# Kernel optimization log

Hardware: AMD Instinct MI355X
Metric: run time of the kernel (lower is better)

Reference implementation:

```python
import jax, jax.numpy as jnp
import numpy as np

D_MODEL = 1024
NUM_HEADS = 16


def setup_inputs() -> dict:
    key = jax.random.key(0)
    ks = jax.random.split(key, 9)
    B, S, D = 4, 1024, D_MODEL
    scale = 1.0 / np.sqrt(D)
    inp = {
        "query": jax.random.normal(ks[0], (B, S, D), dtype=jnp.float32),
        "key": jax.random.normal(ks[1], (B, S, D), dtype=jnp.float32),
        "value": jax.random.normal(ks[2], (B, S, D), dtype=jnp.float32),
        # causal mask: 1 = attend, 0 = blocked (masked_fill where mask==0)
        "mask": jnp.tril(jnp.ones((S, S), dtype=jnp.int32))[None, None, :, :],
        "Wq": jax.random.normal(ks[3], (D, D), dtype=jnp.float32) * scale,
        "Wk": jax.random.normal(ks[4], (D, D), dtype=jnp.float32) * scale,
        "Wv": jax.random.normal(ks[5], (D, D), dtype=jnp.float32) * scale,
        "Wo": jax.random.normal(ks[6], (D, D), dtype=jnp.float32) * scale,
        "bo": jnp.zeros((D,), dtype=jnp.float32),
    }
    return inp


def reference(query, key, value, mask, Wq, Wk, Wv, Wo, bo):
    B, S, D = query.shape
    H = NUM_HEADS
    dk = D // H
    # torch Linear: y = x @ W.T  (bias=False for q/k/v)
    def proj(x, W):
        return (x @ W.T).reshape(B, S, H, dk).transpose(0, 2, 1, 3)  # [B,H,S,dk]

    Q = proj(query, Wq)
    K = proj(key, Wk)
    V = proj(value, Wv)

    scores = jnp.einsum("bhqd,bhkd->bhqk", Q, K) / jnp.sqrt(
        jnp.asarray(dk, dtype=jnp.float32)
    )
    scores = jnp.where(mask == 0, jnp.asarray(-1e9, scores.dtype), scores)
    attn = jax.nn.softmax(scores, axis=-1)
    out = jnp.einsum("bhqk,bhkd->bhqd", attn, V)  # [B,H,S,dk]
    out = out.transpose(0, 2, 1, 3).reshape(B, S, D)
    return out @ Wo.T + bo
```

## Files before the change

### kernel.cpp

```cpp
#include <hip/hip_runtime.h>

typedef __bf16 bf16x8 __attribute__((ext_vector_type(8)));
typedef short  s16x8  __attribute__((ext_vector_type(8)));
typedef float  f32x4  __attribute__((ext_vector_type(4)));
typedef float  f32x16 __attribute__((ext_vector_type(16)));
typedef unsigned int   u32x4 __attribute__((ext_vector_type(4)));
typedef unsigned short u16x4 __attribute__((ext_vector_type(4)));

#define NH   16
#define HD   64
#define SEQ  1024
#define DM   1024
#define NB   4
#define MTOT 4096

#define SCALE_L2E 0.1803368801111204f

__device__ __forceinline__ unsigned short f2bf(float f) {
    unsigned u = __builtin_bit_cast(unsigned, f);
    u += 0x7FFFu + ((u >> 16) & 1u);
    return (unsigned short)(u >> 16);
}

__device__ __forceinline__ s16x8 cvt8(f32x4 a, f32x4 b) {
    s16x8 r;
    r[0] = (short)f2bf(a[0]); r[1] = (short)f2bf(a[1]);
    r[2] = (short)f2bf(a[2]); r[3] = (short)f2bf(a[3]);
    r[4] = (short)f2bf(b[0]); r[5] = (short)f2bf(b[1]);
    r[6] = (short)f2bf(b[2]); r[7] = (short)f2bf(b[3]);
    return r;
}

__device__ __forceinline__ unsigned short bfbits(float x) {
    __bf16 h = (__bf16)x;
    return __builtin_bit_cast(unsigned short, h);
}
__device__ __forceinline__ float bf2f(unsigned short b) {
    unsigned u = (unsigned)b << 16;
    return __builtin_bit_cast(float, u);
}
__device__ __forceinline__ unsigned pk2(float a, float b) {
    return (unsigned)bfbits(a) | ((unsigned)bfbits(b) << 16);
}

__device__ __forceinline__ void gl16(const void* g, void* l) {
    __builtin_amdgcn_global_load_lds(
        (const __attribute__((address_space(1))) unsigned int*)g,
        (__attribute__((address_space(3))) unsigned int*)l, 16, 0, 0);
}

__global__ __launch_bounds__(256)
void cvt_kernel(const float* __restrict__ q, const float* __restrict__ k,
                const float* __restrict__ v, const float* __restrict__ wq,
                const float* __restrict__ wk, const float* __restrict__ wv,
                const float* __restrict__ wo,
                unsigned short* __restrict__ dq, unsigned short* __restrict__ dk,
                unsigned short* __restrict__ dv, unsigned short* __restrict__ dwq,
                unsigned short* __restrict__ dwk, unsigned short* __restrict__ dwv,
                unsigned short* __restrict__ dwo)
{
    const int id = blockIdx.x;
    const float* s; unsigned short* d; int off; float scl = 1.0f;
    if (id < 6144) {
        const int t = id >> 11; off = id & 2047;
        s = (t == 0) ? q : (t == 1) ? k : v;
        d = (t == 0) ? dq : (t == 1) ? dk : dv;
    } else {
        const int w = (id - 6144) >> 9; off = (id - 6144) & 511;
        s = (w == 0) ? wq : (w == 1) ? wk : (w == 2) ? wv : wo;
        d = (w == 0) ? dwq : (w == 1) ? dwk : (w == 2) ? dwv : dwo;
        if (w == 0) scl = SCALE_L2E;
    }
    const int idx = off * 2048 + threadIdx.x * 8;
    const f32x4* sp = (const f32x4*)(s + idx);
    *(s16x8*)(d + idx) = cvt8(sp[0] * scl, sp[1] * scl);
}

__device__ __forceinline__ void stage128x64(const unsigned short* __restrict__ src,
                                            int row0, int k0, char* lds, int tid)
{
    const int wv  = tid >> 6;
    const int row = tid >> 3;
    const int scx = ((tid & 7) * 16) ^ ((row & 7) << 4);
    #pragma unroll
    for (int i = 0; i < 4; ++i) {
        const char* g = (const char*)(src + (size_t)(row0 + i * 32 + row) * DM + k0) + scx;
        gl16(g, lds + i * 4096 + wv * 1024);
    }
}

__device__ __forceinline__ void stage_half(const unsigned short* __restrict__ src,
                                           int grow0, int k0, char* ldsdst, int tid)
{
    const int wv  = tid >> 6;
    const int row = tid >> 3;
    const int scx = ((tid & 7) * 16) ^ ((row & 7) << 4);
    gl16((const char*)(src + (size_t)(grow0 + row) * DM + k0) + scx,
         ldsdst + wv * 1024);
    gl16((const char*)(src + (size_t)(grow0 + 64 + row) * DM + k0) + scx,
         ldsdst + 8192 + wv * 1024);
}

__device__ __forceinline__ bf16x8 ldfrag(const char* base, int row, int cb) {
    return __builtin_bit_cast(bf16x8,
        *(const s16x8*)(base + row * 128 + (cb ^ ((row & 7) << 4))));
}

__global__ __launch_bounds__(512, 2)
void proj_kernel(const unsigned short* __restrict__ Xq,
                 const unsigned short* __restrict__ Xk,
                 const unsigned short* __restrict__ Xv,
                 const unsigned short* __restrict__ Wq,
                 const unsigned short* __restrict__ Wk,
                 const unsigned short* __restrict__ Wv,
                 unsigned short* __restrict__ Qo, unsigned short* __restrict__ Ko,
                 unsigned short* __restrict__ VTo)
{
    __shared__ char smem[147456];

    const int bid = blockIdx.x;
    const int swz = (bid & 7) * 24 + (bid >> 3);
    const int which = swz >> 6;
    const int rem   = swz & 63;
    const int m0 = (rem >> 2) * 256, n0 = (rem & 3) * 256;

    const unsigned short* X = (which == 0) ? Xq : (which == 1) ? Xk : Xv;
    const unsigned short* W = (which == 0) ? Wq : (which == 1) ? Wk : Wv;

    const int tid = threadIdx.x, lane = tid & 63, wv = tid >> 6;
    const int wrB = (wv >> 2) * 128;
    const int wcB = (wv & 3) * 64;
    const int fr = lane & 15, hi = lane >> 4, r4 = hi * 4;

    f32x4 acc[8][4];
    #pragma unroll
    for (int i = 0; i < 8; ++i)
        #pragma unroll
        for (int j = 0; j < 4; ++j) acc[i][j] = (f32x4){0.f, 0.f, 0.f, 0.f};

    stage_half(X, m0,       0, smem +     0, tid);
    stage_half(X, m0 + 128, 0, smem + 16384, tid);
    stage_half(W, n0,       0, smem + 32768, tid);
    stage_half(W, n0 + 128, 0, smem + 49152, tid);

    for (int t = 0; t < 16; ++t) {
        const char* Abuf = smem + (t & 1) * 65536;
        const char* Bbuf = Abuf + 32768;
        char* nb = smem + ((t & 1) ^ 1) * 65536;
        const int kn = (t + 1) * 64;

        bf16x8 af[2][4], bf01[2][2], bf23[2][2];

        if (t < 15) {
            stage_half(X, m0, kn, nb, tid);
            asm volatile("s_waitcnt vmcnt(2)" ::: "memory");
        } else {
            asm volatile("s_waitcnt vmcnt(0)" ::: "memory");
        }
        __builtin_amdgcn_s_barrier();
        __builtin_amdgcn_sched_barrier(0);
        #pragma unroll
        for (int ks = 0; ks < 2; ++ks) {
            const int cb = ks * 64 + hi * 16;
            #pragma unroll
            for (int mt = 0; mt < 4; ++mt) af[ks][mt] = ldfrag(Abuf, wrB + mt * 16 + fr, cb);
            #pragma unroll
            for (int nt = 0; nt < 2; ++nt) bf01[ks][nt] = ldfrag(Bbuf, wcB + nt * 16 + fr, cb);
        }
        __builtin_amdgcn_s_setprio(1);
        #pragma unroll
        for (int ks = 0; ks < 2; ++ks)
            #pragma unroll
            for (int mt = 0; mt < 4; ++mt)
                #pragma unroll
                for (int nt = 0; nt < 2; ++nt)
                    acc[mt][nt] = __builtin_amdgcn_mfma_f32_16x16x32_bf16(
                        af[ks][mt], bf01[ks][nt], acc[mt][nt], 0, 0, 0);
        __builtin_amdgcn_s_setprio(0);

        __builtin_amdgcn_s_barrier();
        __builtin_amdgcn_sched_barrier(0);
        #pragma unroll
        for (int ks = 0; ks < 2; ++ks) {
            const int cb = ks * 64 + hi * 16;
            #pragma unroll
            for (int nt = 0; nt < 2; ++nt) bf23[ks][nt] = ldfrag(Bbuf, wcB + 32 + nt * 16 + fr, cb);
        }
        if (t < 15) stage_half(X, m0 + 128, kn, nb + 16384, tid);
        __builtin_amdgcn_s_setprio(1);
        #pragma unroll
        for (int ks = 0; ks < 2; ++ks)
            #pragma unroll
            for (int mt = 0; mt < 4; ++mt)
                #pragma unroll
                for (int nt = 0; nt < 2; ++nt)
                    acc[mt][nt + 2] = __builtin_amdgcn_mfma_f32_16x16x32_bf16(
                        af[ks][mt], bf23[ks][nt], acc[mt][nt + 2], 0, 0, 0);
        __builtin_amdgcn_s_setprio(0);

        __builtin_amdgcn_s_barrier();
        __builtin_amdgcn_sched_barrier(0);
        #pragma unroll
        for (int ks = 0; ks < 2; ++ks) {
            const int cb = ks * 64 + hi * 16;
            #pragma unroll
            for (int mt = 0; mt < 4; ++mt) af[ks][mt] = ldfrag(Abuf, wrB + 64 + mt * 16 + fr, cb);
        }
        if (t < 15) stage_half(W, n0, kn, nb + 32768, tid);
        __builtin_amdgcn_s_setprio(1);
        #pragma unroll
        for (int ks = 0; ks < 2; ++ks)
            #pragma unroll
            for (int mt = 0; mt < 4; ++mt)
                #pragma unroll
                for (int nt = 0; nt < 2; ++nt)
                    acc[mt + 4][nt] = __builtin_amdgcn_mfma_f32_16x16x32_bf16(
                        af[ks][mt], bf01[ks][nt], acc[mt + 4][nt], 0, 0, 0);
        __builtin_amdgcn_s_setprio(0);

        __builtin_amdgcn_s_barrier();
        __builtin_amdgcn_sched_barrier(0);
        if (t < 15) stage_half(W, n0 + 128, kn, nb + 49152, tid);
        __builtin_amdgcn_s_setprio(1);
        #pragma unroll
        for (int ks = 0; ks < 2; ++ks)
            #pragma unroll
            for (int mt = 0; mt < 4; ++mt)
                #pragma unroll
                for (int nt = 0; nt < 2; ++nt)
                    acc[mt + 4][nt + 2] = __builtin_amdgcn_mfma_f32_16x16x32_bf16(
                        af[ks][mt], bf23[ks][nt], acc[mt + 4][nt + 2], 0, 0, 0);
        __builtin_amdgcn_s_setprio(0);
    }

    __syncthreads();

    unsigned short* sE = (unsigned short*)(smem + wv * 18432);
    #pragma unroll
    for (int mt = 0; mt < 8; ++mt)
        #pragma unroll
        for (int nt = 0; nt < 4; ++nt)
            #pragma unroll
            for (int r = 0; r < 4; ++r) {
                const int row = mt * 16 + r4 + r;
                const int col = nt * 16 + fr;
                sE[row * 72 + (col ^ (((row >> 3) & 7) << 3))] = f2bf(acc[mt][nt][r]);
            }
    asm volatile("s_waitcnt lgkmcnt(0)" ::: "memory");

    const int hB    = (n0 + wcB) >> 6;
    const int sbase = m0 + wrB;
    const int bb    = sbase >> 10;
    const int srow0 = sbase & 1023;

    if (which < 2) {
        unsigned short* QK = ((which == 0) ? Qo : Ko)
            + (((size_t)(bb * NH + hB)) * SEQ + srow0) * HD;
        #pragma unroll
        for (int it = 0; it < 16; ++it) {
            const int idx = it * 64 + lane;
            const int row = idx >> 3, c = idx & 7;
            s16x8 v = *(const s16x8*)&sE[row * 72 + ((c ^ ((row >> 3) & 7)) * 8)];
            *(s16x8*)(QK + (size_t)row * HD + c * 8) = v;
        }
    } else {
        const int t0 = srow0 >> 6;
        unsigned short* VD = VTo + (size_t)(bb * NH + hB) * (SEQ * HD)
                                 + (size_t)t0 * 4096;
        #pragma unroll
        for (int it = 0; it < 16; ++it) {
            const int tt = it >> 3, r = it & 7;
            const int sb = tt * 64 + (r >> 1) * 16 + (lane >> 5) * 8;
            const int d  = (lane & 31) + (r & 1) * 32;
            s16x8 v;
            #pragma unroll
            for (int j = 0; j < 8; ++j) {
                const int row = sb + j;
                v[j] = (short)sE[row * 72 + (d ^ (((row >> 3) & 7) << 3))];
            }
            *(s16x8*)(VD + (size_t)(tt * 8 + r) * 512 + lane * 8) = v;
        }
    }
}

#define GEMM_K_LOOP(SRC_A, SRC_B)                                              \
    stage128x64(SRC_A, m0, 0, sA[0], tid);                                     \
    stage128x64(SRC_B, n0, 0, sB[0], tid);                                     \
    for (int kt = 0; kt < 16; ++kt) {                                          \
        const int cur = kt & 1;                                                \
        if (kt < 15) {                                                         \
            stage128x64(SRC_A, m0, (kt + 1) * 64, sA[cur ^ 1], tid);           \
            stage128x64(SRC_B, n0, (kt + 1) * 64, sB[cur ^ 1], tid);           \
            asm volatile("s_waitcnt vmcnt(8)" ::: "memory");                   \
        } else {                                                               \
            asm volatile("s_waitcnt vmcnt(0)" ::: "memory");                   \
        }                                                                      \
        __builtin_amdgcn_s_barrier();                                          \
        __builtin_amdgcn_sched_barrier(0);                                     \
        _Pragma("unroll")                                                      \
        for (int ks = 0; ks < 2; ++ks) {                                       \
            const int cb = ks * 64 + hi * 16;                                  \
            bf16x8 af[4], bfm[4];                                              \
            _Pragma("unroll")                                                  \
            for (int mt = 0; mt < 4; ++mt)                                     \
                af[mt] = ldfrag(sA[cur], wr + mt * 16 + fr, cb);               \
            _Pragma("unroll")                                                  \
            for (int nt = 0; nt < 4; ++nt)                                     \
                bfm[nt] = ldfrag(sB[cur], wc + nt * 16 + fr, cb);              \
            _Pragma("unroll")                                                  \
            for (int mt = 0; mt < 4; ++mt)                                     \
                _Pragma("unroll")                                              \
                for (int nt = 0; nt < 4; ++nt)                                 \
                    acc[mt][nt] = __builtin_amdgcn_mfma_f32_16x16x32_bf16(     \
                        af[mt], bfm[nt], acc[mt][nt], 0, 0, 0);                \
        }                                                                      \
        asm volatile("s_waitcnt lgkmcnt(0)" ::: "memory");                     \
        __builtin_amdgcn_sched_barrier(0);                                     \
        __builtin_amdgcn_s_barrier();                                          \
    }

__global__ __launch_bounds__(256)
void outproj_kernel(const unsigned short* __restrict__ A,
                    const unsigned short* __restrict__ Wo,
                    const float* __restrict__ bo,
                    float* __restrict__ Cout)
{
    const int bid = blockIdx.x;
    const int swz = (bid & 7) * 32 + (bid >> 3);
    const int m0 = (swz >> 3) * 128, n0 = (swz & 7) * 128;

    __shared__ char sA[2][16384];
    __shared__ char sB[2][16384];

    const int tid = threadIdx.x, lane = tid & 63, wv = tid >> 6;
    const int wr = (wv >> 1) * 64, wc = (wv & 1) * 64;
    const int fr = lane & 15, hi = lane >> 4, r4 = hi * 4;

    f32x4 acc[4][4];
    #pragma unroll
    for (int i = 0; i < 4; ++i)
        #pragma unroll
        for (int j = 0; j < 4; ++j) acc[i][j] = (f32x4){0.f, 0.f, 0.f, 0.f};

    GEMM_K_LOOP(A, Wo)

    #pragma unroll
    for (int mt = 0; mt < 4; ++mt)
        #pragma unroll
        for (int nt = 0; nt < 4; ++nt)
            #pragma unroll
            for (int r = 0; r < 4; ++r) {
                int gm = m0 + wr + mt * 16 + r4 + r;
                int gn = n0 + wc + nt * 16 + fr;
                Cout[(size_t)gm * DM + gn] = acc[mt][nt][r] + bo[gn];
            }
}

__device__ __forceinline__ void stageK64(const char* Kc, int t, char* myK, int lane) {
    const int krow8 = lane >> 3;
    const int kcol  = ((lane & 7) * 16) ^ (krow8 << 4);
    const char* kb = Kc + (size_t)t * 8192;
    #pragma unroll
    for (int i = 0; i < 8; ++i)
        gl16(kb + (i * 8 + krow8) * 128 + kcol, myK + i * 1024);
}

__global__ __launch_bounds__(256)
void attn_kernel(const unsigned short* __restrict__ Q,
                 const unsigned short* __restrict__ K,
                 const unsigned short* __restrict__ VT,
                 unsigned short* __restrict__ O)
{
    __shared__ char smem[4][8192];

    const int bid = blockIdx.x;
    const int xcd = bid & 7, idx = bid >> 3;
    const int bh  = xcd * 8 + (idx & 7);
    const int rb  = 15 - (idx >> 3);
    const int tid = threadIdx.x, lane = tid & 63, wv = tid >> 6;
    const int g = wv >> 1, p = wv & 1;
    const int q0w = rb * 64 + g * 32;
    const int ql = lane & 31, hi = lane >> 5;
    const int qg = q0w + ql;
    const int ndiag = q0w >> 6;

    char* myK = smem[wv];

    const unsigned short* Qp = Q + (size_t)bh * SEQ * HD;
    const char* Kc  = (const char*)(K  + (size_t)bh * SEQ * HD);
    const char* Vfc = (const char*)(VT + (size_t)bh * SEQ * HD);

    bf16x8 qf[4];
    #pragma unroll
    for (int s = 0; s < 4; ++s)
        qf[s] = __builtin_bit_cast(bf16x8,
            *(const s16x8*)(Qp + (size_t)qg * HD + s * 16 + hi * 8));

    f32x16 o0, o1;
    #pragma unroll
    for (int i = 0; i < 16; ++i) { o0[i] = 0.f; o1[i] = 0.f; }
    float mrow = -3.0e38f, lrow = 0.f;

    if (p <= ndiag) stageK64(Kc, p, myK, lane);

    for (int t = p; t <= ndiag; t += 2) {
        asm volatile("s_waitcnt vmcnt(0)" ::: "memory");
        __builtin_amdgcn_sched_barrier(0);

        f32x16 s0, s1;
        #pragma unroll
        for (int i = 0; i < 16; ++i) { s0[i] = 0.f; s1[i] = 0.f; }
        #pragma unroll
        for (int s = 0; s < 4; ++s) {
            const int cb = s * 32 + hi * 16;
            bf16x8 k0 = ldfrag(myK, ql, cb);
            bf16x8 k1 = ldfrag(myK, 32 + ql, cb);
            s0 = __builtin_amdgcn_mfma_f32_32x32x16_bf16(k0, qf[s], s0, 0, 0, 0);
            s1 = __builtin_amdgcn_mfma_f32_32x32x16_bf16(k1, qf[s], s1, 0, 0, 0);
        }
        asm volatile("s_waitcnt lgkmcnt(0)" ::: "memory");
        __builtin_amdgcn_sched_barrier(0);

        const char* vb = Vfc + (size_t)t * 8192;
        s16x8 vr[8];
        #pragma unroll
        for (int r = 0; r < 8; ++r)
            vr[r] = *(const s16x8*)(vb + r * 1024 + lane * 16);
        if (t + 2 <= ndiag) stageK64(Kc, t + 2, myK, lane);

        if (t == ndiag) {
            #pragma unroll
            for (int r = 0; r < 16; ++r) {
                const int kl = t * 64 + (r & 3) + 8 * (r >> 2) + 4 * hi;
                s0[r] = (kl      <= qg) ? s0[r] : -3.0e38f;
                s1[r] = (kl + 32 <= qg) ? s1[r] : -3.0e38f;
            }
        }

        float mt = s0[0];
        #pragma unroll
        for (int r = 1; r < 16; ++r) mt = fmaxf(mt, s0[r]);
        #pragma unroll
        for (int r = 0; r < 16; ++r) mt = fmaxf(mt, s1[r]);
        mt = fmaxf(mt, __shfl_xor(mt, 32, 64));

        if (!__all(mt - mrow <= 8.0f)) {
            const float mnew = fmaxf(mrow, mt);
            const float pc = __builtin_amdgcn_exp2f(mrow - mnew);
            mrow = mnew;
            lrow *= pc;
            #pragma unroll
            for (int i = 0; i < 16; ++i) { o0[i] *= pc; o1[i] *= pc; }
        }

        float ts = 0.f;
        #pragma unroll
        for (int r = 0; r < 16; ++r) { s0[r] = __builtin_amdgcn_exp2f(s0[r] - mrow); ts += s0[r]; }
        #pragma unroll
        for (int r = 0; r < 16; ++r) { s1[r] = __builtin_amdgcn_exp2f(s1[r] - mrow); ts += s1[r]; }
        ts += __shfl_xor(ts, 32, 64);
        lrow += ts;

        #pragma unroll
        for (int s = 0; s < 4; ++s) {
            const f32x16 ps = (s < 2) ? s0 : s1;
            const int bse = (s & 1) * 8;
            unsigned w0 = pk2(ps[bse + 0], ps[bse + 1]);
            unsigned w1 = pk2(ps[bse + 2], ps[bse + 3]);
            unsigned w2 = pk2(ps[bse + 4], ps[bse + 5]);
            unsigned w3 = pk2(ps[bse + 6], ps[bse + 7]);
            unsigned x0 = (unsigned)__shfl_xor((int)(hi ? w0 : w2), 32, 64);
            unsigned x1 = (unsigned)__shfl_xor((int)(hi ? w1 : w3), 32, 64);
            u32x4 fw;
            fw[0] = hi ? x0 : w0;
            fw[1] = hi ? x1 : w1;
            fw[2] = hi ? w2 : x0;
            fw[3] = hi ? w3 : x1;
            const bf16x8 pfrag = __builtin_bit_cast(bf16x8, fw);
            o0 = __builtin_amdgcn_mfma_f32_32x32x16_bf16(
                __builtin_bit_cast(bf16x8, vr[2 * s]), pfrag, o0, 0, 0, 0);
            o1 = __builtin_amdgcn_mfma_f32_32x32x16_bf16(
                __builtin_bit_cast(bf16x8, vr[2 * s + 1]), pfrag, o1, 0, 0, 0);
        }
    }

    if (p == 1) {
        unsigned* rec = (unsigned*)smem[wv] + lane * 21;
        #pragma unroll
        for (int i = 0; i < 8; ++i) rec[i]     = pk2(o0[2 * i], o0[2 * i + 1]);
        #pragma unroll
        for (int i = 0; i < 8; ++i) rec[8 + i] = pk2(o1[2 * i], o1[2 * i + 1]);
        rec[16] = __builtin_bit_cast(unsigned, mrow);
        rec[17] = __builtin_bit_cast(unsigned, lrow);
        asm volatile("s_waitcnt lgkmcnt(0)" ::: "memory");
    }
    __syncthreads();
    if (p == 0) {
        const unsigned* rec = (const unsigned*)smem[wv + 1] + lane * 21;
        const float m1 = __builtin_bit_cast(float, rec[16]);
        const float l1 = __builtin_bit_cast(float, rec[17]);
        const float ms = fmaxf(mrow, m1);
        const float c0 = __builtin_amdgcn_exp2f(mrow - ms);
        const float c1 = __builtin_amdgcn_exp2f(m1 - ms);
        const float inv = 1.0f / (lrow * c0 + l1 * c1);
        const float a0 = c0 * inv, a1 = c1 * inv;

        unsigned short* sE = (unsigned short*)smem[wv];
        #pragma unroll
        for (int dt = 0; dt < 2; ++dt) {
            const f32x16 ov = dt ? o1 : o0;
            #pragma unroll
            for (int j = 0; j < 4; ++j) {
                u16x4 w;
                #pragma unroll
                for (int i = 0; i < 4; ++i) {
                    const int ii = 4 * j + i;
                    const unsigned uw = rec[dt * 8 + (ii >> 1)];
                    const float pv = bf2f((unsigned short)((ii & 1) ? (uw >> 16) : (uw & 0xffff)));
                    w[i] = bfbits(ov[ii] * a0 + pv * a1);
                }
                *(u16x4*)&sE[ql * 72 + dt * 32 + 8 * j + 4 * hi] = w;
            }
        }
        asm volatile("s_waitcnt lgkmcnt(0)" ::: "memory");
        const int bb = bh >> 4, h = bh & 15;
        #pragma unroll
        for (int it = 0; it < 4; ++it) {
            const int ix = it * 64 + lane;
            const int qq = ix >> 3, c = ix & 7;
            s16x8 v = *(const s16x8*)&sE[qq * 72 + c * 8];
            *(s16x8*)(O + ((size_t)(bb * SEQ + q0w + qq) * DM + h * 64) + c * 8) = v;
        }
    }
}

extern "C" void kernel_launch(void* const* d_in, const int* in_sizes, int n_in,
                              void* d_out, int out_size, void* d_ws, size_t ws_size,
                              hipStream_t stream)
{
    const float* query = (const float*)d_in[0];
    const float* key   = (const float*)d_in[1];
    const float* value = (const float*)d_in[2];
    const float* Wq = (const float*)d_in[4];
    const float* Wk = (const float*)d_in[5];
    const float* Wv = (const float*)d_in[6];
    const float* Wo = (const float*)d_in[7];
    const float* bo = (const float*)d_in[8];
    float* out = (float*)d_out;

    const size_t XE = (size_t)MTOT * DM;
    const size_t WE = (size_t)DM * DM;
    unsigned short* ws16 = (unsigned short*)d_ws;
    unsigned short* Xq16 = ws16;
    unsigned short* Xk16 = Xq16 + XE;
    unsigned short* Xv16 = Xk16 + XE;
    unsigned short* Wq16 = Xv16 + XE;
    unsigned short* Wk16 = Wq16 + WE;
    unsigned short* Wv16 = Wk16 + WE;
    unsigned short* Wo16 = Wv16 + WE;
    unsigned short* Qw   = Wo16 + WE;
    unsigned short* Kw   = Qw + XE;
    unsigned short* VTw  = Kw + XE;
    unsigned short* AO   = VTw + XE;

    cvt_kernel<<<dim3(8192), dim3(256), 0, stream>>>(
        query, key, value, Wq, Wk, Wv, Wo,
        Xq16, Xk16, Xv16, Wq16, Wk16, Wv16, Wo16);

    proj_kernel<<<dim3(192), dim3(512), 0, stream>>>(
        Xq16, Xk16, Xv16, Wq16, Wk16, Wv16, Qw, Kw, VTw);

    attn_kernel<<<dim3(1024), dim3(256), 0, stream>>>(Qw, Kw, VTw, AO);

    outproj_kernel<<<dim3(256), dim3(256), 0, stream>>>(AO, Wo16, bo, out);
}
```

Baseline: 94.79 us.

## Fuse fp32-to-bf16 conversion into projection and output GEMM tile loads

Removes the standalone conversion kernel. The projection and output-projection GEMMs now read fp32 inputs and weights directly through registers, convert them to bf16 and write them into swizzled LDS, with the Q scale folded into the weight conversion. This drops a full write and re-read of bf16 copies plus one kernel launch. In exchange, the asynchronous global-to-LDS loads become register-staged loads with more VGPR pressure. Each GEMM tile also reads twice the bytes, and the weights are re-converted by every block.

```diff
diff --git a/kernel.cpp b/kernel.cpp
--- a/kernel.cpp
+++ b/kernel.cpp
@@ -49,31 +49,49 @@
         (__attribute__((address_space(3))) unsigned int*)l, 16, 0, 0);
 }
 
-__global__ __launch_bounds__(256)
-void cvt_kernel(const float* __restrict__ q, const float* __restrict__ k,
-                const float* __restrict__ v, const float* __restrict__ wq,
-                const float* __restrict__ wk, const float* __restrict__ wv,
-                const float* __restrict__ wo,
-                unsigned short* __restrict__ dq, unsigned short* __restrict__ dk,
-                unsigned short* __restrict__ dv, unsigned short* __restrict__ dwq,
-                unsigned short* __restrict__ dwk, unsigned short* __restrict__ dwv,
-                unsigned short* __restrict__ dwo)
-{
-    const int id = blockIdx.x;
-    const float* s; unsigned short* d; int off; float scl = 1.0f;
-    if (id < 6144) {
-        const int t = id >> 11; off = id & 2047;
-        s = (t == 0) ? q : (t == 1) ? k : v;
-        d = (t == 0) ? dq : (t == 1) ? dk : dv;
-    } else {
-        const int w = (id - 6144) >> 9; off = (id - 6144) & 511;
-        s = (w == 0) ? wq : (w == 1) ? wk : (w == 2) ? wv : wo;
-        d = (w == 0) ? dwq : (w == 1) ? dwk : (w == 2) ? dwv : dwo;
-        if (w == 0) scl = SCALE_L2E;
-    }
-    const int idx = off * 2048 + threadIdx.x * 8;
-    const f32x4* sp = (const f32x4*)(s + idx);
-    *(s16x8*)(d + idx) = cvt8(sp[0] * scl, sp[1] * scl);
+__device__ __forceinline__ bf16x8 ldfrag(const char* base, int row, int cb) {
+    return __builtin_bit_cast(bf16x8,
+        *(const s16x8*)(base + row * 128 + (cb ^ ((row & 7) << 4))));
+}
+
+__device__ __forceinline__ void loadH512(const float* __restrict__ src, int grow0,
+                                         int k0, int tid, f32x4 v[4])
+{
+    const int row = tid >> 3;
+    const int ce  = (tid & 7) * 8;
+    const f32x4* p0 = (const f32x4*)(src + (size_t)(grow0 + row) * DM + k0 + ce);
+    v[0] = p0[0]; v[1] = p0[1];
+    const f32x4* p1 = (const f32x4*)(src + (size_t)(grow0 + 64 + row) * DM + k0 + ce);
+    v[2] = p1[0]; v[3] = p1[1];
+}
+__device__ __forceinline__ void writeH512(char* dst, int tid, const f32x4 v[4], float scl)
+{
+    const int row = tid >> 3;
+    const int cB  = (tid & 7) * 16;
+    *(s16x8*)(dst + row * 128 + (cB ^ ((row & 7) << 4))) = cvt8(v[0] * scl, v[1] * scl);
+    const int r2 = row + 64;
+    *(s16x8*)(dst + r2 * 128 + (cB ^ ((r2 & 7) << 4))) = cvt8(v[2] * scl, v[3] * scl);
+}
+
+__device__ __forceinline__ void loadB256(const float* __restrict__ src, int row0,
+                                         int k0, int tid, f32x4 v[8])
+{
+    const int ce = (tid & 7) * 8;
+    #pragma unroll
+    for (int i = 0; i < 4; ++i) {
+        const int row = (tid >> 3) + i * 32;
+        const f32x4* p = (const f32x4*)(src + (size_t)(row0 + row) * DM + k0 + ce);
+        v[2 * i] = p[0]; v[2 * i + 1] = p[1];
+    }
+}
+__device__ __forceinline__ void writeB256(char* dst, int tid, const f32x4 v[8])
+{
+    const int cB = (tid & 7) * 16;
+    #pragma unroll
+    for (int i = 0; i < 4; ++i) {
+        const int row = (tid >> 3) + i * 32;
+        *(s16x8*)(dst + row * 128 + (cB ^ ((row & 7) << 4))) = cvt8(v[2 * i], v[2 * i + 1]);
+    }
 }
 
 __device__ __forceinline__ void stage128x64(const unsigned short* __restrict__ src,
@@ -89,30 +107,10 @@
     }
 }
 
-__device__ __forceinline__ void stage_half(const unsigned short* __restrict__ src,
-                                           int grow0, int k0, char* ldsdst, int tid)
-{
-    const int wv  = tid >> 6;
-    const int row = tid >> 3;
-    const int scx = ((tid & 7) * 16) ^ ((row & 7) << 4);
-    gl16((const char*)(src + (size_t)(grow0 + row) * DM + k0) + scx,
-         ldsdst + wv * 1024);
-    gl16((const char*)(src + (size_t)(grow0 + 64 + row) * DM + k0) + scx,
-         ldsdst + 8192 + wv * 1024);
-}
-
-__device__ __forceinline__ bf16x8 ldfrag(const char* base, int row, int cb) {
-    return __builtin_bit_cast(bf16x8,
-        *(const s16x8*)(base + row * 128 + (cb ^ ((row & 7) << 4))));
-}
-
 __global__ __launch_bounds__(512, 2)
-void proj_kernel(const unsigned short* __restrict__ Xq,
-                 const unsigned short* __restrict__ Xk,
-                 const unsigned short* __restrict__ Xv,
-                 const unsigned short* __restrict__ Wq,
-                 const unsigned short* __restrict__ Wk,
-                 const unsigned short* __restrict__ Wv,
+void proj_kernel(const float* __restrict__ Xq, const float* __restrict__ Xk,
+                 const float* __restrict__ Xv, const float* __restrict__ Wq,
+                 const float* __restrict__ Wk, const float* __restrict__ Wv,
                  unsigned short* __restrict__ Qo, unsigned short* __restrict__ Ko,
                  unsigned short* __restrict__ VTo)
 {
@@ -124,8 +122,9 @@
     const int rem   = swz & 63;
     const int m0 = (rem >> 2) * 256, n0 = (rem & 3) * 256;
 
-    const unsigned short* X = (which == 0) ? Xq : (which == 1) ? Xk : Xv;
-    const unsigned short* W = (which == 0) ? Wq : (which == 1) ? Wk : Wv;
+    const float* X = (which == 0) ? Xq : (which == 1) ? Xk : Xv;
+    const float* W = (which == 0) ? Wq : (which == 1) ? Wk : Wv;
+    const float wscl = (which == 0) ? SCALE_L2E : 1.0f;
 
     const int tid = threadIdx.x, lane = tid & 63, wv = tid >> 6;
     const int wrB = (wv >> 2) * 128;
@@ -138,10 +137,14 @@
         #pragma unroll
         for (int j = 0; j < 4; ++j) acc[i][j] = (f32x4){0.f, 0.f, 0.f, 0.f};
 
-    stage_half(X, m0,       0, smem +     0, tid);
-    stage_half(X, m0 + 128, 0, smem + 16384, tid);
-    stage_half(W, n0,       0, smem + 32768, tid);
-    stage_half(W, n0 + 128, 0, smem + 49152, tid);
+    {
+        f32x4 v[4];
+        loadH512(X, m0,       0, tid, v); writeH512(smem +     0, tid, v, 1.0f);
+        loadH512(X, m0 + 128, 0, tid, v); writeH512(smem + 16384, tid, v, 1.0f);
+        loadH512(W, n0,       0, tid, v); writeH512(smem + 32768, tid, v, wscl);
+        loadH512(W, n0 + 128, 0, tid, v); writeH512(smem + 49152, tid, v, wscl);
+    }
+    __syncthreads();
 
     for (int t = 0; t < 16; ++t) {
         const char* Abuf = smem + (t & 1) * 65536;
@@ -150,15 +153,9 @@
         const int kn = (t + 1) * 64;
 
         bf16x8 af[2][4], bf01[2][2], bf23[2][2];
-
-        if (t < 15) {
-            stage_half(X, m0, kn, nb, tid);
-            asm volatile("s_waitcnt vmcnt(2)" ::: "memory");
-        } else {
-            asm volatile("s_waitcnt vmcnt(0)" ::: "memory");
-        }
-        __builtin_amdgcn_s_barrier();
-        __builtin_amdgcn_sched_barrier(0);
+        f32x4 h0[4], h1[4], h2[4], h3[4];
+
+        if (t < 15) loadH512(X, m0, kn, tid, h0);
         #pragma unroll
         for (int ks = 0; ks < 2; ++ks) {
             const int cb = ks * 64 + hi * 16;
@@ -186,7 +183,7 @@
             #pragma unroll
             for (int nt = 0; nt < 2; ++nt) bf23[ks][nt] = ldfrag(Bbuf, wcB + 32 + nt * 16 + fr, cb);
         }
-        if (t < 15) stage_half(X, m0 + 128, kn, nb + 16384, tid);
+        if (t < 15) { loadH512(X, m0 + 128, kn, tid, h1); writeH512(nb, tid, h0, 1.0f); }
         __builtin_amdgcn_s_setprio(1);
         #pragma unroll
         for (int ks = 0; ks < 2; ++ks)
@@ -206,7 +203,7 @@
             #pragma unroll
             for (int mt = 0; mt < 4; ++mt) af[ks][mt] = ldfrag(Abuf, wrB + 64 + mt * 16 + fr, cb);
         }
-        if (t < 15) stage_half(W, n0, kn, nb + 32768, tid);
+        if (t < 15) { loadH512(W, n0, kn, tid, h2); writeH512(nb + 16384, tid, h1, 1.0f); }
         __builtin_amdgcn_s_setprio(1);
         #pragma unroll
         for (int ks = 0; ks < 2; ++ks)
@@ -220,7 +217,7 @@
 
         __builtin_amdgcn_s_barrier();
         __builtin_amdgcn_sched_barrier(0);
-        if (t < 15) stage_half(W, n0 + 128, kn, nb + 49152, tid);
+        if (t < 15) { loadH512(W, n0 + 128, kn, tid, h3); writeH512(nb + 32768, tid, h2, wscl); }
         __builtin_amdgcn_s_setprio(1);
         #pragma unroll
         for (int ks = 0; ks < 2; ++ks)
@@ -231,6 +228,10 @@
                     acc[mt + 4][nt + 2] = __builtin_amdgcn_mfma_f32_16x16x32_bf16(
                         af[ks][mt], bf23[ks][nt], acc[mt + 4][nt + 2], 0, 0, 0);
         __builtin_amdgcn_s_setprio(0);
+        if (t < 15) writeH512(nb + 49152, tid, h3, wscl);
+        asm volatile("s_waitcnt lgkmcnt(0)" ::: "memory");
+        __builtin_amdgcn_sched_barrier(0);
+        __builtin_amdgcn_s_barrier();
     }
 
     __syncthreads();
@@ -283,45 +284,9 @@
     }
 }
 
-#define GEMM_K_LOOP(SRC_A, SRC_B)                                              \
-    stage128x64(SRC_A, m0, 0, sA[0], tid);                                     \
-    stage128x64(SRC_B, n0, 0, sB[0], tid);                                     \
-    for (int kt = 0; kt < 16; ++kt) {                                          \
-        const int cur = kt & 1;                                                \
-        if (kt < 15) {                                                         \
-            stage128x64(SRC_A, m0, (kt + 1) * 64, sA[cur ^ 1], tid);           \
-            stage128x64(SRC_B, n0, (kt + 1) * 64, sB[cur ^ 1], tid);           \
-            asm volatile("s_waitcnt vmcnt(8)" ::: "memory");                   \
-        } else {                                                               \
-            asm volatile("s_waitcnt vmcnt(0)" ::: "memory");                   \
-        }                                                                      \
-        __builtin_amdgcn_s_barrier();                                          \
-        __builtin_amdgcn_sched_barrier(0);                                     \
-        _Pragma("unroll")                                                      \
-        for (int ks = 0; ks < 2; ++ks) {                                       \
-            const int cb = ks * 64 + hi * 16;                                  \
-            bf16x8 af[4], bfm[4];                                              \
-            _Pragma("unroll")                                                  \
-            for (int mt = 0; mt < 4; ++mt)                                     \
-                af[mt] = ldfrag(sA[cur], wr + mt * 16 + fr, cb);               \
-            _Pragma("unroll")                                                  \
-            for (int nt = 0; nt < 4; ++nt)                                     \
-                bfm[nt] = ldfrag(sB[cur], wc + nt * 16 + fr, cb);              \
-            _Pragma("unroll")                                                  \
-            for (int mt = 0; mt < 4; ++mt)                                     \
-                _Pragma("unroll")                                              \
-                for (int nt = 0; nt < 4; ++nt)                                 \
-                    acc[mt][nt] = __builtin_amdgcn_mfma_f32_16x16x32_bf16(     \
-                        af[mt], bfm[nt], acc[mt][nt], 0, 0, 0);                \
-        }                                                                      \
-        asm volatile("s_waitcnt lgkmcnt(0)" ::: "memory");                     \
-        __builtin_amdgcn_sched_barrier(0);                                     \
-        __builtin_amdgcn_s_barrier();                                          \
-    }
-
 __global__ __launch_bounds__(256)
 void outproj_kernel(const unsigned short* __restrict__ A,
-                    const unsigned short* __restrict__ Wo,
+                    const float* __restrict__ Wo,
                     const float* __restrict__ bo,
                     float* __restrict__ Cout)
 {
@@ -342,7 +307,45 @@
         #pragma unroll
         for (int j = 0; j < 4; ++j) acc[i][j] = (f32x4){0.f, 0.f, 0.f, 0.f};
 
-    GEMM_K_LOOP(A, Wo)
+    f32x4 bv[8];
+    loadB256(Wo, n0, 0, tid, bv);
+    stage128x64(A, m0, 0, sA[0], tid);
+    writeB256(sB[0], tid, bv);
+    __syncthreads();
+
+    for (int kt = 0; kt < 16; ++kt) {
+        const int cur = kt & 1;
+        if (kt < 15) {
+            loadB256(Wo, n0, (kt + 1) * 64, tid, bv);
+            stage128x64(A, m0, (kt + 1) * 64, sA[cur ^ 1], tid);
+            asm volatile("s_waitcnt vmcnt(12)" ::: "memory");
+        } else {
+            asm volatile("s_waitcnt vmcnt(0)" ::: "memory");
+        }
+        __builtin_amdgcn_s_barrier();
+        __builtin_amdgcn_sched_barrier(0);
+        #pragma unroll
+        for (int ks = 0; ks < 2; ++ks) {
+            const int cb = ks * 64 + hi * 16;
+            bf16x8 af[4], bfm[4];
+            #pragma unroll
+            for (int mt = 0; mt < 4; ++mt)
+                af[mt] = ldfrag(sA[cur], wr + mt * 16 + fr, cb);
+            #pragma unroll
+            for (int nt = 0; nt < 4; ++nt)
+                bfm[nt] = ldfrag(sB[cur], wc + nt * 16 + fr, cb);
+            #pragma unroll
+            for (int mt = 0; mt < 4; ++mt)
+                #pragma unroll
+                for (int nt = 0; nt < 4; ++nt)
+                    acc[mt][nt] = __builtin_amdgcn_mfma_f32_16x16x32_bf16(
+                        af[mt], bfm[nt], acc[mt][nt], 0, 0, 0);
+        }
+        if (kt < 15) writeB256(sB[cur ^ 1], tid, bv);
+        asm volatile("s_waitcnt lgkmcnt(0)" ::: "memory");
+        __builtin_amdgcn_sched_barrier(0);
+        __builtin_amdgcn_s_barrier();
+    }
 
     #pragma unroll
     for (int mt = 0; mt < 4; ++mt)
@@ -549,28 +552,16 @@
     float* out = (float*)d_out;
 
     const size_t XE = (size_t)MTOT * DM;
-    const size_t WE = (size_t)DM * DM;
     unsigned short* ws16 = (unsigned short*)d_ws;
-    unsigned short* Xq16 = ws16;
-    unsigned short* Xk16 = Xq16 + XE;
-    unsigned short* Xv16 = Xk16 + XE;
-    unsigned short* Wq16 = Xv16 + XE;
-    unsigned short* Wk16 = Wq16 + WE;
-    unsigned short* Wv16 = Wk16 + WE;
-    unsigned short* Wo16 = Wv16 + WE;
-    unsigned short* Qw   = Wo16 + WE;
+    unsigned short* Qw   = ws16;
     unsigned short* Kw   = Qw + XE;
     unsigned short* VTw  = Kw + XE;
     unsigned short* AO   = VTw + XE;
 
-    cvt_kernel<<<dim3(8192), dim3(256), 0, stream>>>(
-        query, key, value, Wq, Wk, Wv, Wo,
-        Xq16, Xk16, Xv16, Wq16, Wk16, Wv16, Wo16);
-
     proj_kernel<<<dim3(192), dim3(512), 0, stream>>>(
-        Xq16, Xk16, Xv16, Wq16, Wk16, Wv16, Qw, Kw, VTw);
+        query, key, value, Wq, Wk, Wv, Qw, Kw, VTw);
 
     attn_kernel<<<dim3(1024), dim3(256), 0, stream>>>(Qw, Kw, VTw, AO);
 
-    outproj_kernel<<<dim3(256), dim3(256), 0, stream>>>(AO, Wo16, bo, out);
-}
+    outproj_kernel<<<dim3(256), dim3(256), 0, stream>>>(AO, Wo, bo, out);
+}
```

Measured after the change: 95.81 us. No clear change (+1.1%).
